# Kernel optimization log

Hardware: AMD Instinct MI355X
Metric: run time of the kernel (lower is better)

Reference implementation:

```python
import jax, jax.numpy as jnp
import numpy as np

NUM_CLASSES = 81
THRESHOLD = 0.5
NEGPOS_RATIO = 3
OBJ_SCORE = 0.01
VAR0, VAR1 = 0.1, 0.2


def point_form(boxes):
    # center form (cx,cy,w,h) -> corner form (x1,y1,x2,y2)
    return jnp.concatenate([boxes[:, :2] - boxes[:, 2:] / 2,
                            boxes[:, :2] + boxes[:, 2:] / 2], axis=1)


def jaccard(a, b):
    # a: [A,4] corners, b: [B,4] corners -> IoU [A,B]
    lt = jnp.maximum(a[:, None, :2], b[None, :, :2])
    rb = jnp.minimum(a[:, None, 2:], b[None, :, 2:])
    wh = jnp.clip(rb - lt, 0.0)
    inter = wh[..., 0] * wh[..., 1]
    area_a = ((a[:, 2] - a[:, 0]) * (a[:, 3] - a[:, 1]))[:, None]
    area_b = ((b[:, 2] - b[:, 0]) * (b[:, 3] - b[:, 1]))[None, :]
    return inter / (area_a + area_b - inter)


def encode(matched, priors):
    # matched: [P,4] corner-form GT, priors: [P,4] center-form
    g_cxcy = ((matched[:, :2] + matched[:, 2:]) / 2 - priors[:, :2]) / (VAR0 * priors[:, 2:])
    g_wh = jnp.log((matched[:, 2:] - matched[:, :2]) / priors[:, 2:]) / VAR1
    return jnp.concatenate([g_cxcy, g_wh], axis=1)


def match_one(truths, labels, priors):
    # truths: [O,4] corners, labels: [O] int, priors: [P,4] center-form
    overlaps = jaccard(truths, point_form(priors))      # [O,P]
    best_prior_idx = jnp.argmax(overlaps, axis=1)       # [O]
    best_truth_overlap = jnp.max(overlaps, axis=0)      # [P]
    best_truth_idx = jnp.argmax(overlaps, axis=0)       # [P]
    # ensure every gt matches its best prior
    best_truth_overlap = best_truth_overlap.at[best_prior_idx].set(2.0)
    best_truth_idx = best_truth_idx.at[best_prior_idx].set(jnp.arange(truths.shape[0]))
    matches = truths[best_truth_idx]                    # [P,4]
    conf = jnp.where(best_truth_overlap < THRESHOLD, 0, labels[best_truth_idx].astype(jnp.int32))
    return encode(matches, priors), conf


def smooth_l1(x):
    ax = jnp.abs(x)
    return jnp.where(ax < 1.0, 0.5 * ax * ax, ax - 0.5)


def ce_per_row(logits, tgt):
    # sum-reduction cross-entropy components: logsumexp - logit[target]
    lse = jax.nn.logsumexp(logits, axis=-1)
    picked = jnp.take_along_axis(logits, tgt[..., None].astype(jnp.int32), axis=-1)[..., 0]
    return lse - picked


def setup_inputs() -> dict:
    key = jax.random.key(0)
    ks = jax.random.split(key, 8)
    B, P, O, C = 32, 24564, 16, NUM_CLASSES
    loc_data = jax.random.normal(ks[0], (B, P, 4), jnp.float32)
    conf_data = jax.random.normal(ks[1], (B, P, C), jnp.float32)
    obj_data = jax.random.normal(ks[2], (B, P, 2), jnp.float32)
    # priors in center form
    pc = jax.random.uniform(ks[3], (P, 2), jnp.float32, 0.0, 1.0)
    pwh = jax.random.uniform(ks[4], (P, 2), jnp.float32, 0.05, 0.5)
    priors = jnp.concatenate([pc, pwh], axis=1)
    # gt boxes in corner form, valid (x1<x2, y1<y2)
    tc = jax.random.uniform(ks[5], (B, O, 2), jnp.float32, 0.2, 0.8)
    twh = jax.random.uniform(ks[6], (B, O, 2), jnp.float32, 0.05, 0.3)
    truths = jnp.concatenate([jnp.clip(tc - twh / 2, 0.0, 1.0),
                              jnp.clip(tc + twh / 2, 0.0, 1.0)], axis=-1)
    labels = jax.random.randint(ks[7], (B, O), 1, C).astype(jnp.int64)
    return {"loc_data": loc_data, "conf_data": conf_data, "obj_data": obj_data,
            "priors": priors, "truths": truths, "labels": labels}


def reference(loc_data, conf_data, obj_data, priors, truths, labels):
    num, num_priors = loc_data.shape[:2]
    loc_t, conf_t = jax.vmap(match_one, in_axes=(0, 0, None))(truths, labels, priors)
    loc_t = jax.lax.stop_gradient(loc_t)      # Variable(requires_grad=False)
    conf_t = jax.lax.stop_gradient(conf_t)
    obj_t = (conf_t > 0).astype(jnp.int32)

    obj_conf = jax.lax.stop_gradient(obj_data[:, :, 1])   # .detach()
    pos = conf_t > 0
    # faithful to original (buggy) filter: (pos + neg_positive) > 2 is never true
    neg_positive = (pos.astype(jnp.int32) + (obj_conf < OBJ_SCORE).astype(jnp.int32)) > 2
    pos = pos & ~neg_positive
    pos = jnp.where(pos.sum() == 0, conf_t > 0, pos)

    # localization loss (smooth L1, sum over positives)
    l1 = smooth_l1(loc_data - loc_t).sum(-1)               # [B,P]
    loss_l = jnp.sum(jnp.where(pos, l1, 0.0))

    # objectness loss with hard negative mining
    ce_obj = ce_per_row(obj_data, obj_t)                   # [B,P]
    pos_obj = obj_t > 0
    mining_obj = jnp.where(pos_obj, 0.0, jax.lax.stop_gradient(ce_obj))
    rank_obj = jnp.argsort(jnp.argsort(-mining_obj, axis=1), axis=1)
    num_obj_pos = pos_obj.sum(1, keepdims=True)
    num_obj_neg = jnp.minimum(NEGPOS_RATIO * num_obj_pos, num_priors - 1)
    neg_obj = rank_obj < num_obj_neg
    loss_obj = jnp.sum(jnp.where(pos_obj | neg_obj, ce_obj, 0.0))

    # class confidence loss with hard negative mining
    ce_c = ce_per_row(conf_data, conf_t)                   # [B,P]
    mining_c = jnp.where(pos, 0.0, jax.lax.stop_gradient(ce_c))
    rank_c = jnp.argsort(jnp.argsort(-mining_c, axis=1), axis=1)
    num_pos = pos.sum(1, keepdims=True)
    num_neg = jnp.minimum(NEGPOS_RATIO * num_pos, num_priors - 1)
    neg = rank_c < num_neg
    loss_c = jnp.sum(jnp.where(pos | neg, ce_c, 0.0))

    N = jnp.maximum(num_pos.sum(), 1).astype(loc_data.dtype)
    N1 = jnp.maximum(num_obj_neg.sum(), 1).astype(loc_data.dtype)
    return (loss_l / N, loss_c / N, 0.4 * loss_obj / N1)
```

## Files before the change

kernel.cpp:

```cpp
#include <hip/hip_runtime.h>
#include <hip/hip_bf16.h>
#include <math.h>

#define BB 32
#define PP 24564
#define OO 16
#define CC 81
#define BP (BB * PP)
#define CHUNK 1024

typedef unsigned long long ull;

__device__ __forceinline__ float sl1(float x) {
    float ax = fabsf(x);
    return ax < 1.0f ? 0.5f * ax * ax : ax - 0.5f;
}

__global__ __launch_bounds__(256) void k_match_a(
        const float* __restrict__ priors, const float* __restrict__ truths,
        float* __restrict__ bto, int* __restrict__ bti,
        ull* __restrict__ best_prior ) {
    const int b = blockIdx.y;
    const int p0 = blockIdx.x * CHUNK;
    const int tid = threadIdx.x;
    __shared__ float tr[OO][4];
    __shared__ float tarea[OO];
    __shared__ ull red[OO];
    if (tid < OO * 4) ((float*)tr)[tid] = truths[b * OO * 4 + tid];
    if (tid < OO) red[tid] = 0ull;
    __syncthreads();
    if (tid < OO) tarea[tid] = (tr[tid][2] - tr[tid][0]) * (tr[tid][3] - tr[tid][1]);
    __syncthreads();

    float bpv[OO];
    int bpi[OO];
#pragma unroll
    for (int o = 0; o < OO; o++) { bpv[o] = -1.0f; bpi[o] = -1; }

    const int pend = (p0 + CHUNK < PP) ? p0 + CHUNK : PP;
    for (int p = p0 + tid; p < pend; p += 256) {
        const float4 pr = ((const float4*)priors)[p];
        const float x1 = pr.x - pr.z * 0.5f, y1 = pr.y - pr.w * 0.5f;
        const float x2 = pr.x + pr.z * 0.5f, y2 = pr.y + pr.w * 0.5f;
        const float parea = (x2 - x1) * (y2 - y1);
        float best = -1.0f;
        int bidx = 0;
#pragma unroll
        for (int o = 0; o < OO; o++) {
            const float lx = fmaxf(tr[o][0], x1), ly = fmaxf(tr[o][1], y1);
            const float rx = fminf(tr[o][2], x2), ry = fminf(tr[o][3], y2);
            const float iw = fmaxf(rx - lx, 0.0f), ih = fmaxf(ry - ly, 0.0f);
            const float inter = iw * ih;
            const float iou = inter / (tarea[o] + parea - inter);
            if (iou > best) { best = iou; bidx = o; }
            if (iou > bpv[o]) { bpv[o] = iou; bpi[o] = p; }
        }
        bto[(size_t)b * PP + p] = best;
        bti[(size_t)b * PP + p] = bidx;
    }

#pragma unroll
    for (int o = 0; o < OO; o++) {
        if (bpi[o] >= 0) {
            const ull key = ((ull)__float_as_uint(bpv[o]) << 32) |
                            (ull)(0xFFFFFFFFu - (unsigned)bpi[o]);
            atomicMax(&red[o], key);
        }
    }
    __syncthreads();
    if (tid < OO && red[tid] != 0ull)
        atomicMax(&best_prior[b * OO + tid], red[tid]);
}

__global__ void k_match_b(const ull* __restrict__ best_prior,
                          float* __restrict__ bto, int* __restrict__ bti) {
    const int b = threadIdx.x;
    if (b >= BB) return;
    for (int o = 0; o < OO; o++) {
        const unsigned p = 0xFFFFFFFFu - (unsigned)(best_prior[b * OO + o] & 0xFFFFFFFFull);
        bto[(size_t)b * PP + p] = 2.0f;
        bti[(size_t)b * PP + p] = o;
    }
}

__global__ __launch_bounds__(256) void k_ce(
        const float* __restrict__ conf, const float* __restrict__ obj,
        const float* __restrict__ loc, const float* __restrict__ priors,
        const float* __restrict__ truths, const int* __restrict__ labels,
        const float* __restrict__ bto, const int* __restrict__ bti,
        float* __restrict__ mining_obj, float* __restrict__ mining_c,
        int* __restrict__ num_posS ,
        float* __restrict__ accS  ) {
    const int tid = threadIdx.x;
    const int row0 = blockIdx.x * 64;
    __shared__ float sconf[64 * CC];
    __shared__ float slse[64];

    const float4* src = (const float4*)(conf + (size_t)row0 * CC);
    float4* dst = (float4*)sconf;
    for (int i = tid; i < (64 * CC) / 4; i += 256) dst[i] = src[i];
    __syncthreads();

    const int r = tid >> 2;
    const int part = tid & 3;
    const float* rowp = sconf + r * CC;
    const int c0 = part * 20;
    const int c1 = (part == 3) ? CC : c0 + 20;
    float m = -INFINITY;
    for (int c = c0; c < c1; c++) m = fmaxf(m, rowp[c]);
    m = fmaxf(m, __shfl_xor(m, 1));
    m = fmaxf(m, __shfl_xor(m, 2));
    float s = 0.0f;
    for (int c = c0; c < c1; c++) s += __expf(rowp[c] - m);
    s += __shfl_xor(s, 1);
    s += __shfl_xor(s, 2);
    if (part == 0) slse[r] = m + __logf(s);
    __syncthreads();

    if (tid < 64) {
        const int row = row0 + tid;
        const int b = row / PP;
        const int p = row - b * PP;
        const float ov = bto[row];
        const int ti = bti[row];
        const int lbl = labels[b * OO + ti];
        const int tgt = (ov < 0.5f) ? 0 : lbl;
        const float ce_c = slse[tid] - sconf[tid * CC + tgt];

        const float2 o2 = ((const float2*)obj)[row];
        const float mo = fmaxf(o2.x, o2.y);
        const float lse_o = mo + __logf(__expf(o2.x - mo) + __expf(o2.y - mo));
        const bool pos = tgt > 0;
        const float ce_o = lse_o - (pos ? o2.y : o2.x);

        mining_c[row]   = pos ? 0.0f : ce_c;
        mining_obj[row] = pos ? 0.0f : ce_o;

        float my_l = 0.0f, my_co = 0.0f, my_cc = 0.0f;
        if (pos) {
            my_co = ce_o;
            my_cc = ce_c;
            const float4 pr = ((const float4*)priors)[p];
            const float4 t  = ((const float4*)truths)[b * OO + ti];
            const float gcx = ((t.x + t.z) * 0.5f - pr.x) / (0.1f * pr.z);
            const float gcy = ((t.y + t.w) * 0.5f - pr.y) / (0.1f * pr.w);
            const float gw = logf((t.z - t.x) / pr.z) / 0.2f;
            const float gh = logf((t.w - t.y) / pr.w) / 0.2f;
            const float4 ld = ((const float4*)loc)[row];
            my_l = sl1(ld.x - gcx) + sl1(ld.y - gcy) +
                   sl1(ld.z - gw) + sl1(ld.w - gh);
        }

        const int b0 = row0 / PP;
        const ull mpos = __ballot(pos);
        const ull mb1  = __ballot(b != b0);
#pragma unroll
        for (int d = 32; d; d >>= 1) {
            my_l  += __shfl_down(my_l,  d);
            my_co += __shfl_down(my_co, d);
            my_cc += __shfl_down(my_cc, d);
        }
        if (tid == 0 && mpos) {
            const int cnt0 = __popcll(mpos & ~mb1);
            const int cnt1 = __popcll(mpos &  mb1);
            int* nps = num_posS + (blockIdx.x & 7) * BB;
            if (cnt0) atomicAdd(&nps[b0], cnt0);
            if (cnt1) atomicAdd(&nps[b0 + 1], cnt1);
            float* slot = accS + (size_t)(blockIdx.x & 63) * 32;
            atomicAdd(slot + 0, my_l);
            atomicAdd(slot + 1, my_co);
            atomicAdd(slot + 2, my_cc);
        }
    }
}

__global__ __launch_bounds__(256) void k_select(
        const float* __restrict__ mining ,
        const int* __restrict__ num_posS ,
        float* __restrict__ acc,
        int* __restrict__ n1_acc) {
    const int arr = blockIdx.x >> 5;
    const int b = blockIdx.x & 31;
    const float* x = mining + ((size_t)arr * BB + b) * PP;
    int np = 0;
#pragma unroll
    for (int s = 0; s < 8; s++) np += num_posS[s * BB + b];
    long long k64 = 3LL * np;
    const int k = (int)(k64 < (long long)(PP - 1) ? k64 : (long long)(PP - 1));
    if (threadIdx.x == 0 && arr == 0) atomicAdd(n1_acc, k);
    if (k <= 0) return;

    __shared__ unsigned hist[256];
    __shared__ unsigned s_prefix;
    __shared__ int s_krem;
    if (threadIdx.x == 0) { s_prefix = 0u; s_krem = k; }
    __syncthreads();

    for (int shift = 24; shift >= 0; shift -= 8) {
        hist[threadIdx.x] = 0u;
        __syncthreads();
        const unsigned prefix = s_prefix;
        const unsigned pmask = (shift == 24) ? 0u : (0xFFFFFFFFu << (shift + 8));
        for (int i = threadIdx.x; i < PP; i += 256) {
            const unsigned u = __float_as_uint(x[i]);
            if ((u & pmask) == prefix)
                atomicAdd(&hist[(u >> shift) & 255u], 1u);
        }
        __syncthreads();
        if (threadIdx.x == 0) {
            const int krem = s_krem;
            unsigned cum = 0;
            int sel = 0;
            for (int byte = 255; byte >= 0; byte--) {
                const unsigned h = hist[byte];
                if (cum + h >= (unsigned)krem) { sel = byte; break; }
                cum += h;
            }
            s_krem = krem - (int)cum;
            s_prefix = prefix | ((unsigned)sel << shift);
        }
        __syncthreads();
    }

    const unsigned t = s_prefix;
    float lsum = 0.0f;
    unsigned lcnt = 0;
    for (int i = threadIdx.x; i < PP; i += 256) {
        const float v = x[i];
        if (__float_as_uint(v) > t) { lsum += v; lcnt++; }
    }
    __shared__ float sred[256];
    __shared__ unsigned cred[256];
    sred[threadIdx.x] = lsum;
    cred[threadIdx.x] = lcnt;
    __syncthreads();
    for (int st = 128; st; st >>= 1) {
        if (threadIdx.x < st) {
            sred[threadIdx.x] += sred[threadIdx.x + st];
            cred[threadIdx.x] += cred[threadIdx.x + st];
        }
        __syncthreads();
    }
    if (threadIdx.x == 0) {
        const float tsum = sred[0] + (float)(k - (int)cred[0]) * __uint_as_float(t);
        atomicAdd(&acc[3 + arr], tsum);
    }
}

__global__ void k_final(const float* __restrict__ acc,
                        const float* __restrict__ accS ,
                        const int* __restrict__ num_posS ,
                        const int* __restrict__ n1_acc,
                        float* __restrict__ out) {
    const int t = threadIdx.x;
    float sl = accS[t * 32 + 0];
    float so = accS[t * 32 + 1];
    float sc = accS[t * 32 + 2];
    int np = 0;
#pragma unroll
    for (int i = 0; i < 4; i++) np += num_posS[t + i * 64];
#pragma unroll
    for (int d = 32; d; d >>= 1) {
        sl += __shfl_down(sl, d);
        so += __shfl_down(so, d);
        sc += __shfl_down(sc, d);
        np += __shfl_down(np, d);
    }
    if (t == 0) {
        const float fN = (float)(np > 1 ? np : 1);
        const int n1 = *n1_acc;
        const float fN1 = (float)(n1 > 1 ? n1 : 1);
        out[0] = sl / fN;
        out[1] = (sc + acc[4]) / fN;
        out[2] = 0.4f * (so + acc[3]) / fN1;
    }
}

extern "C" void kernel_launch(void* const* d_in, const int* in_sizes, int n_in,
                              void* d_out, int out_size, void* d_ws, size_t ws_size,
                              hipStream_t stream) {
    const float* loc_data  = (const float*)d_in[0];
    const float* conf_data = (const float*)d_in[1];
    const float* obj_data  = (const float*)d_in[2];
    const float* priors    = (const float*)d_in[3];
    const float* truths    = (const float*)d_in[4];
    const int*   labels    = (const int*)d_in[5];
    float* out = (float*)d_out;

    float* ws_f = (float*)d_ws;
    float* bto = ws_f;
    int*   bti = (int*)(ws_f + BP);
    float* mining = ws_f + 2 * (size_t)BP;
    ull*   best_prior = (ull*)(ws_f + 4 * (size_t)BP);
    int*   num_posS = (int*)(ws_f + 4 * (size_t)BP + 1024);
    float* acc = ws_f + 4 * (size_t)BP + 1280;
    int*   n1_acc = (int*)(ws_f + 4 * (size_t)BP + 1288);
    float* accS = ws_f + 4 * (size_t)BP + 2048;

    hipMemsetAsync((void*)best_prior, 0, 16384, stream);

    dim3 mg((PP + CHUNK - 1) / CHUNK, BB);
    k_match_a<<<mg, 256, 0, stream>>>(priors, truths, bto, bti, best_prior);
    k_match_b<<<1, 32, 0, stream>>>(best_prior, bto, bti);

    k_ce<<<BP / 64, 256, 0, stream>>>(conf_data, obj_data, loc_data, priors,
                                      truths, labels, bto, bti,
                                      mining , mining + BP ,
                                      num_posS, accS);

    k_select<<<64, 256, 0, stream>>>(mining, num_posS, acc, n1_acc);

    k_final<<<1, 64, 0, stream>>>(acc, accS, num_posS, n1_acc, out);
}
```

Measured before the change: 563.5 us.

## Widen top-k select blocks to 1024 threads and use wave-shuffle reductions

The radix-select kernel now runs 1024 threads per block instead of 256, so each of the 64 blocks scans its row of 24,564 mining values with four times as many threads. Its shared-memory tree reduction is replaced by wave shuffles plus a 16-entry combine. In the match kernel, the per-prior best-IoU keys are reduced with 64-bit shuffle max within each wave, replacing per-thread shared atomics on 16 slots. Both changes target latency in small-grid kernels, at the cost of more threads contending for the 256-bin histogram atomics.

```diff
diff --git a/kernel.cpp b/kernel.cpp
--- a/kernel.cpp
+++ b/kernel.cpp
@@ -25,9 +25,8 @@
     const int tid = threadIdx.x;
     __shared__ float tr[OO][4];
     __shared__ float tarea[OO];
-    __shared__ ull red[OO];
+    __shared__ ull red[4][OO];
     if (tid < OO * 4) ((float*)tr)[tid] = truths[b * OO * 4 + tid];
-    if (tid < OO) red[tid] = 0ull;
     __syncthreads();
     if (tid < OO) tarea[tid] = (tr[tid][2] - tr[tid][0]) * (tr[tid][3] - tr[tid][1]);
     __syncthreads();
@@ -59,17 +58,30 @@
         bti[(size_t)b * PP + p] = bidx;
     }
 
+    const int wave = tid >> 6;
+    const int lane = tid & 63;
 #pragma unroll
     for (int o = 0; o < OO; o++) {
-        if (bpi[o] >= 0) {
-            const ull key = ((ull)__float_as_uint(bpv[o]) << 32) |
-                            (ull)(0xFFFFFFFFu - (unsigned)bpi[o]);
-            atomicMax(&red[o], key);
-        }
-    }
-    __syncthreads();
-    if (tid < OO && red[tid] != 0ull)
-        atomicMax(&best_prior[b * OO + tid], red[tid]);
+        ull key = (bpi[o] >= 0)
+            ? (((ull)__float_as_uint(bpv[o]) << 32) |
+               (ull)(0xFFFFFFFFu - (unsigned)bpi[o]))
+            : 0ull;
+#pragma unroll
+        for (int d = 32; d; d >>= 1) {
+            const ull other = __shfl_xor(key, d);
+            key = (other > key) ? other : key;
+        }
+        if (lane == 0) red[wave][o] = key;
+    }
+    __syncthreads();
+    if (tid < OO) {
+        const ull k0 = red[0][tid], k1 = red[1][tid];
+        const ull k2 = red[2][tid], k3 = red[3][tid];
+        ull m = k0 > k1 ? k0 : k1;
+        const ull m2 = k2 > k3 ? k2 : k3;
+        m = m > m2 ? m : m2;
+        if (m != 0ull) atomicMax(&best_prior[b * OO + tid], m);
+    }
 }
 
 __global__ void k_match_b(const ull* __restrict__ best_prior,
@@ -174,40 +186,43 @@
     }
 }
 
-__global__ __launch_bounds__(256) void k_select(
+__global__ __launch_bounds__(1024) void k_select(
         const float* __restrict__ mining ,
         const int* __restrict__ num_posS ,
         float* __restrict__ acc,
         int* __restrict__ n1_acc) {
     const int arr = blockIdx.x >> 5;
     const int b = blockIdx.x & 31;
+    const int tid = threadIdx.x;
     const float* x = mining + ((size_t)arr * BB + b) * PP;
     int np = 0;
 #pragma unroll
     for (int s = 0; s < 8; s++) np += num_posS[s * BB + b];
     long long k64 = 3LL * np;
     const int k = (int)(k64 < (long long)(PP - 1) ? k64 : (long long)(PP - 1));
-    if (threadIdx.x == 0 && arr == 0) atomicAdd(n1_acc, k);
+    if (tid == 0 && arr == 0) atomicAdd(n1_acc, k);
     if (k <= 0) return;
 
     __shared__ unsigned hist[256];
     __shared__ unsigned s_prefix;
     __shared__ int s_krem;
-    if (threadIdx.x == 0) { s_prefix = 0u; s_krem = k; }
-    __syncthreads();
+    __shared__ float wsum[16];
+    __shared__ unsigned wcnt[16];
+    if (tid == 0) { s_prefix = 0u; s_krem = k; }
 
     for (int shift = 24; shift >= 0; shift -= 8) {
-        hist[threadIdx.x] = 0u;
         __syncthreads();
+        if (tid < 256) hist[tid] = 0u;
         const unsigned prefix = s_prefix;
         const unsigned pmask = (shift == 24) ? 0u : (0xFFFFFFFFu << (shift + 8));
-        for (int i = threadIdx.x; i < PP; i += 256) {
+        __syncthreads();
+        for (int i = tid; i < PP; i += 1024) {
             const unsigned u = __float_as_uint(x[i]);
             if ((u & pmask) == prefix)
                 atomicAdd(&hist[(u >> shift) & 255u], 1u);
         }
         __syncthreads();
-        if (threadIdx.x == 0) {
+        if (tid == 0) {
             const int krem = s_krem;
             unsigned cum = 0;
             int sel = 0;
@@ -219,30 +234,30 @@
             s_krem = krem - (int)cum;
             s_prefix = prefix | ((unsigned)sel << shift);
         }
-        __syncthreads();
-    }
+    }
+    __syncthreads();
 
     const unsigned t = s_prefix;
     float lsum = 0.0f;
     unsigned lcnt = 0;
-    for (int i = threadIdx.x; i < PP; i += 256) {
+    for (int i = tid; i < PP; i += 1024) {
         const float v = x[i];
         if (__float_as_uint(v) > t) { lsum += v; lcnt++; }
     }
-    __shared__ float sred[256];
-    __shared__ unsigned cred[256];
-    sred[threadIdx.x] = lsum;
-    cred[threadIdx.x] = lcnt;
-    __syncthreads();
-    for (int st = 128; st; st >>= 1) {
-        if (threadIdx.x < st) {
-            sred[threadIdx.x] += sred[threadIdx.x + st];
-            cred[threadIdx.x] += cred[threadIdx.x + st];
-        }
-        __syncthreads();
-    }
-    if (threadIdx.x == 0) {
-        const float tsum = sred[0] + (float)(k - (int)cred[0]) * __uint_as_float(t);
+#pragma unroll
+    for (int d = 32; d; d >>= 1) {
+        lsum += __shfl_down(lsum, d);
+        lcnt += __shfl_down(lcnt, d);
+    }
+    const int wave = tid >> 6;
+    if ((tid & 63) == 0) { wsum[wave] = lsum; wcnt[wave] = lcnt; }
+    __syncthreads();
+    if (tid == 0) {
+        float ts = 0.0f;
+        unsigned tc = 0;
+#pragma unroll
+        for (int w = 0; w < 16; w++) { ts += wsum[w]; tc += wcnt[w]; }
+        const float tsum = ts + (float)(k - (int)tc) * __uint_as_float(t);
         atomicAdd(&acc[3 + arr], tsum);
     }
 }
@@ -308,7 +323,7 @@
                                       mining , mining + BP ,
                                       num_posS, accS);
 
-    k_select<<<64, 256, 0, stream>>>(mining, num_posS, acc, n1_acc);
+    k_select<<<64, 1024, 0, stream>>>(mining, num_posS, acc, n1_acc);
 
     k_final<<<1, 64, 0, stream>>>(acc, accS, num_posS, n1_acc, out);
 }
```

Result: faster. 459.9 us (-18.4%).
